# Optimization experiments

Measured on AMD Instinct MI355X. Metric: run time of the kernel, lower is better.

The kernel has to match this reference:

```python
import jax, jax.numpy as jnp
import numpy as np

B, Z, A = 1024, 512, 8          # batch_size, z_dim, action_dim
AH, ZH = 64, 512                # action_hidden_dim, z_hidden_dim
N_NEG = 100                     # n_neg_actions
TEMP = 0.1                      # temperature
TOP_K = (1, 3, 10)


def forward_model(z, a, Wa, ba, W1, b1, W2, b2):
    # MLP forward model with skip connection (z_delta=True):
    # embed action, concat with z, 2-layer MLP predicting a delta.
    h_a = jax.nn.relu(a @ Wa + ba)                                   # [..., AH]
    h = jax.nn.relu(jnp.concatenate([jnp.broadcast_to(z, a.shape[:-1] + (Z,)), h_a], axis=-1) @ W1 + b1)  # [..., ZH]
    delta = h @ W2 + b2                                              # [..., Z]
    return z + delta


def setup_inputs() -> dict:
    key = jax.random.key(0)
    ks = jax.random.split(key, 8)
    def w(k, shape, fan_in):
        return jax.random.normal(k, shape, jnp.float32) / np.float32(np.sqrt(fan_in))
    z = jax.random.normal(ks[0], (B, Z), jnp.float32)
    z_next = jax.random.normal(ks[1], (B, Z), jnp.float32)
    z_next_hat = jax.random.normal(ks[2], (B, Z), jnp.float32)
    actions = jax.random.normal(ks[3], (B, A), jnp.float32)
    Wa = w(ks[4], (A, AH), A)
    ba = jnp.zeros((AH,), jnp.float32)
    W1 = w(ks[5], (Z + AH, ZH), Z + AH)
    b1 = jnp.zeros((ZH,), jnp.float32)
    W2 = w(ks[6], (ZH, Z), ZH)
    b2 = jnp.zeros((Z,), jnp.float32)
    return {"z": z, "z_next": z_next, "z_next_hat": z_next_hat, "actions": actions,
            "Wa": Wa, "ba": ba, "W1": W1, "b1": b1, "W2": W2, "b2": b2}


def reference(z, z_next, z_next_hat, actions, Wa, ba, W1, b1, W2, b2):
    # ControlCPC.compute_loss with dot_product_similarity, vectorized:
    # the Python loop over n_neg_actions rolled-action forward-model calls
    # becomes one batched [n-1, B, ...] forward-model evaluation.
    batch = z.shape[0]
    n = min(N_NEG, batch)
    sim = z_next @ z_next_hat.T                                      # [B, B] positives on diagonal
    shifts = jnp.arange(1, n)
    neg_actions = jax.vmap(lambda i: jnp.roll(actions, -i, axis=0))(shifts)  # [n-1, B, A]
    z_hat_neg = forward_model(z[None], neg_actions, Wa, ba, W1, b1, W2, b2)  # [n-1, B, Z]
    neg_sim = jnp.einsum('nbz,bz->bn', z_hat_neg, z_next)            # diag of similarity per shift
    sim_mat = jnp.concatenate([sim, neg_sim], axis=1)                # [B, B+n-1]
    # INCE loss, positives on diagonal
    logp = jax.nn.log_softmax(sim_mat / jnp.float32(TEMP), axis=1)
    loss = -jnp.mean(jnp.diagonal(logp))                             # diagonal takes first B entries
    labels = jnp.arange(batch)[:, None]
    accs = []
    for k in TOP_K:
        _, preds = jax.lax.top_k(sim_mat, k)                         # [B, k]
        accs.append(jnp.mean((preds == labels).astype(jnp.float32)) * k)
    return (loss, accs[0], accs[1], accs[2])
```

## Files before the change

kernel.cpp:

```cpp
#include <hip/hip_runtime.h>
#include <math.h>

#define B_SZ 1024
#define Z_DIM 512
#define A_DIM 8
#define AH 64
#define ZH 512
#define NNEG 99
#define INV_T 10.0f

typedef __attribute__((ext_vector_type(8))) short short8;
typedef __attribute__((ext_vector_type(4))) short short4b;
typedef __attribute__((ext_vector_type(4))) float f32x4;

__device__ __forceinline__ short bf16rn(float x) {
    unsigned u = __float_as_uint(x);
    u += 0x7fffu + ((u >> 16) & 1u);
    return (short)(u >> 16);
}
__device__ __forceinline__ void cvt8rn(float4 x0, float4 x1, short8& h) {
    h[0] = bf16rn(x0.x); h[1] = bf16rn(x0.y); h[2] = bf16rn(x0.z); h[3] = bf16rn(x0.w);
    h[4] = bf16rn(x1.x); h[5] = bf16rn(x1.y); h[6] = bf16rn(x1.z); h[7] = bf16rn(x1.w);
}

__device__ __forceinline__ int sw(int m, int kb) { return m * 8 + (kb ^ (m & 7)); }

#define VMWAIT(N) asm volatile("s_waitcnt vmcnt(" #N ")" ::: "memory")
__device__ __forceinline__ void raw_barrier() {
    asm volatile("" ::: "memory");
    __builtin_amdgcn_s_barrier();
    asm volatile("" ::: "memory");
}
typedef const __attribute__((address_space(1))) void* gas_ptr;
typedef __attribute__((address_space(3))) void* las_ptr;
__device__ __forceinline__ void gld_lds16(const void* gsrc, void* ldst) {
    __builtin_amdgcn_global_load_lds((gas_ptr)gsrc, (las_ptr)ldst, 16, 0, 0);
}

__global__ __launch_bounds__(256) void cvt_kernel(
    const float* __restrict__ z, const float* __restrict__ z_next,
    const float* __restrict__ z_next_hat, const float* __restrict__ W1,
    const float* __restrict__ W2, const float* __restrict__ actions,
    const float* __restrict__ Wa, const float* __restrict__ ba,
    short* __restrict__ zb, short* __restrict__ znb, short* __restrict__ znhb,
    short* __restrict__ w1t, short* __restrict__ w2b, short* __restrict__ hab)
{
    const int id = blockIdx.x, tid = threadIdx.x;
    if (id < 896) {
        const float* src; short* dst; int local;
        if (id < 256)      { src = z;          dst = zb;   local = id; }
        else if (id < 512) { src = z_next;     dst = znb;  local = id - 256; }
        else if (id < 768) { src = z_next_hat; dst = znhb; local = id - 512; }
        else               { src = W2;         dst = w2b;  local = id - 768; }
        int i8 = local * 2048 + tid * 8;
        float4 x0 = *(const float4*)&src[i8];
        float4 x1 = *(const float4*)&src[i8 + 4];
        short8 h; cvt8rn(x0, x1, h);
        *(short8*)&dst[i8] = h;
    } else if (id < 968) {
        __shared__ float L[64][68];
        int local = id - 896, kt = local >> 3, nt = local & 7;
#pragma unroll
        for (int i = 0; i < 4; ++i) {
            int f = tid + i * 256;
            int r = f >> 4, c4 = (f & 15) << 2;
            *(float4*)&L[r][c4] = *(const float4*)&W1[(kt * 64 + r) * 512 + nt * 64 + c4];
        }
        __syncthreads();
#pragma unroll
        for (int i = 0; i < 4; ++i) {
            int f = tid + i * 256;
            int r = f >> 4, c4 = (f & 15) << 2;
            short4b o = {bf16rn(L[c4][r]), bf16rn(L[c4 + 1][r]),
                         bf16rn(L[c4 + 2][r]), bf16rn(L[c4 + 3][r])};
            *(short4b*)&w1t[(nt * 64 + r) * 576 + kt * 64 + c4] = o;
        }
    } else {
        __shared__ float sWa[A_DIM * 64];
        __shared__ float sba[64];
        int j0 = (id - 968) * 64;
        for (int i = tid; i < A_DIM * 64; i += 256) sWa[i] = Wa[i];
        if (tid < 64) sba[tid] = ba[tid];
        __syncthreads();
        int r = tid >> 2, c0 = (tid & 3) * 16;
        float4 a0 = *(const float4*)&actions[(j0 + r) * A_DIM + 0];
        float4 a1 = *(const float4*)&actions[(j0 + r) * A_DIM + 4];
        float av[8] = {a0.x, a0.y, a0.z, a0.w, a1.x, a1.y, a1.z, a1.w};
        float o[16];
#pragma unroll
        for (int c = 0; c < 16; ++c) o[c] = sba[c0 + c];
#pragma unroll
        for (int k = 0; k < A_DIM; ++k)
#pragma unroll
            for (int c = 0; c < 16; ++c) o[c] += av[k] * sWa[k * 64 + c0 + c];
#pragma unroll
        for (int c = 0; c < 16; c += 4) {
            short4b h = {bf16rn(fmaxf(o[c], 0.f)),     bf16rn(fmaxf(o[c + 1], 0.f)),
                         bf16rn(fmaxf(o[c + 2], 0.f)), bf16rn(fmaxf(o[c + 3], 0.f))};
            *(short4b*)&hab[(j0 + r) * 64 + c0 + c] = h;
        }
    }
}

__global__ __launch_bounds__(256, 2) void mm_kernel(
    const short* __restrict__ zb, const short* __restrict__ znb,
    const short* __restrict__ znhb, const short* __restrict__ w1t,
    const short* __restrict__ w2b, const short* __restrict__ hab,
    const float* __restrict__ b1,
    float* __restrict__ sim, float* __restrict__ u, float* __restrict__ v,
    float* __restrict__ g)
{
    __shared__ __align__(16) short Ah[128 * 64], Bh[128 * 64];

    const int id = blockIdx.x;
    const int tid = threadIdx.x;

    const short* A; const short* B; const float* bias = nullptr;
    float* C; int N, K, lda, ldb, bm0, bn0;
    if (id < 64) {
        bm0 = (id >> 3) * 128; bn0 = (id & 7) * 128;
        A = znb; lda = 512; B = znhb; ldb = 512; C = sim; N = 1024; K = 512;
    } else if (id < 96) {
        int t = id - 64; bm0 = (t >> 2) * 128; bn0 = (t & 3) * 128;
        A = zb; lda = 512; B = w1t; ldb = 576; C = u; N = 512; K = 512; bias = b1;
    } else if (id < 128) {
        int t = id - 96; bm0 = (t >> 2) * 128; bn0 = (t & 3) * 128;
        A = znb; lda = 512; B = w2b; ldb = 512; C = v; N = 512; K = 512;
    } else {
        int t = id - 128; bm0 = (t >> 2) * 128; bn0 = (t & 3) * 128;
        A = hab; lda = 64; B = w1t + 512; ldb = 576; C = g; N = 512; K = 64;
    }

    const int lane = tid & 63, wv = tid >> 6;
    const int lm = lane & 15, lq = lane >> 4;
    const int wr = (wv >> 1) * 64, wc = (wv & 1) * 64;
    short8* A8 = (short8*)Ah; short8* B8 = (short8*)Bh;
    f32x4 acc[4][4] = {};

    for (int k0 = 0; k0 < K; k0 += 64) {
#pragma unroll
        for (int q = 0; q < 4; ++q) {
            int f = q * 256 + tid;
            int row = f >> 3;
            int ug = (f & 7) ^ (row & 7);
            gld_lds16(&A[(bm0 + row) * lda + k0 + ug * 8],
                      &Ah[(q * 256 + wv * 64) * 8]);
            gld_lds16(&B[(bn0 + row) * ldb + k0 + ug * 8],
                      &Bh[(q * 256 + wv * 64) * 8]);
        }
        VMWAIT(0);
        raw_barrier();
#pragma unroll
        for (int kk = 0; kk < 64; kk += 32) {
            int kbi = (kk >> 3) + lq;
            short8 ah[4], bh[4];
#pragma unroll
            for (int i = 0; i < 4; ++i) ah[i] = A8[sw(wr + i * 16 + lm, kbi)];
#pragma unroll
            for (int j = 0; j < 4; ++j) bh[j] = B8[sw(wc + j * 16 + lm, kbi)];
#pragma unroll
            for (int i = 0; i < 4; ++i)
#pragma unroll
                for (int j = 0; j < 4; ++j)
                    acc[i][j] = __builtin_amdgcn_mfma_f32_16x16x32_bf16(ah[i], bh[j], acc[i][j], 0, 0, 0);
        }
        raw_barrier();
    }
#pragma unroll
    for (int i = 0; i < 4; ++i)
#pragma unroll
        for (int j = 0; j < 4; ++j) {
            int n = bn0 + wc + j * 16 + lm;
            float bb = bias ? bias[n] : 0.0f;
#pragma unroll
            for (int r = 0; r < 4; ++r) {
                int m = bm0 + wr + i * 16 + lq * 4 + r;
                C[m * N + n] = acc[i][j][r] + bb;
            }
        }
}

#define LOADC(GA, GB, kk) { \
    const int q0_ = (kk) * 8; \
    _Pragma("unroll") \
    for (int c_ = 0; c_ < 8; ++c_) { \
        int j_ = (b + 1 + q0_ + c_) & (B_SZ - 1); \
        GA[c_] = *(const float4*)&g[j_ * 512 + lane * 4]; \
        GB[c_] = *(const float4*)&g[j_ * 512 + 256 + lane * 4]; \
    } }

#define LOADC3(GA, GB) { \
    _Pragma("unroll") \
    for (int c_ = 0; c_ < 3; ++c_) { \
        int j_ = (b + 97 + c_) & (B_SZ - 1); \
        GA[c_] = *(const float4*)&g[j_ * 512 + lane * 4]; \
        GB[c_] = *(const float4*)&g[j_ * 512 + 256 + lane * 4]; \
    } }

#define DOTC(T, GA, GB, NC) { \
    _Pragma("unroll") \
    for (int c_ = 0; c_ < (NC); ++c_) { \
        float s_ = 0.0f; \
        s_ += fmaxf(ua.x + GA[c_].x, 0.0f) * va.x; \
        s_ += fmaxf(ua.y + GA[c_].y, 0.0f) * va.y; \
        s_ += fmaxf(ua.z + GA[c_].z, 0.0f) * va.z; \
        s_ += fmaxf(ua.w + GA[c_].w, 0.0f) * va.w; \
        s_ += fmaxf(ub.x + GB[c_].x, 0.0f) * vb.x; \
        s_ += fmaxf(ub.y + GB[c_].y, 0.0f) * vb.y; \
        s_ += fmaxf(ub.z + GB[c_].z, 0.0f) * vb.z; \
        s_ += fmaxf(ub.w + GB[c_].w, 0.0f) * vb.w; \
        T[c_] = s_; \
    } }

#define REDST(T, kk, NC) { \
    for (int off_ = 32; off_; off_ >>= 1) { \
        _Pragma("unroll") \
        for (int c_ = 0; c_ < (NC); ++c_) T[c_] += __shfl_down(T[c_], off_); \
    } \
    if (lane == 0) { \
        _Pragma("unroll") \
        for (int c_ = 0; c_ < (NC); ++c_) rn[(kk) * 8 + c_] = c0 + T[c_]; \
    } }

__global__ __launch_bounds__(256, 2) void row2_kernel(
    const float* __restrict__ sim, const float* __restrict__ u,
    const float* __restrict__ v, const float* __restrict__ g,
    const float* __restrict__ z, const float* __restrict__ z_next,
    const float* __restrict__ b2,
    float* __restrict__ pw)
{
    const int b = blockIdx.x;
    const int tid = threadIdx.x;
    const int w = tid >> 6, lane = tid & 63;
    __shared__ float rn[104];
    __shared__ float sred[12];

    float4 ua = *(const float4*)&u[b * 512 + lane * 4];
    float4 ub = *(const float4*)&u[b * 512 + 256 + lane * 4];
    float4 va = *(const float4*)&v[b * 512 + lane * 4];
    float4 vb = *(const float4*)&v[b * 512 + 256 + lane * 4];
    float4 s4 = *(const float4*)&sim[b * 1024 + tid * 4];
    float diag = sim[b * 1024 + b];

    float p;
    {
        float4 za = *(const float4*)&z[b * 512 + lane * 4];
        float4 zb4 = *(const float4*)&z[b * 512 + 256 + lane * 4];
        float4 na = *(const float4*)&z_next[b * 512 + lane * 4];
        float4 nb = *(const float4*)&z_next[b * 512 + 256 + lane * 4];
        float4 ca = *(const float4*)&b2[lane * 4];
        float4 cb = *(const float4*)&b2[256 + lane * 4];
        p  = (za.x + ca.x) * na.x + (za.y + ca.y) * na.y + (za.z + ca.z) * na.z + (za.w + ca.w) * na.w;
        p += (zb4.x + cb.x) * nb.x + (zb4.y + cb.y) * nb.y + (zb4.z + cb.z) * nb.z + (zb4.w + cb.w) * nb.w;
    }
    for (int off = 32; off; off >>= 1) p += __shfl_down(p, off);
    const float c0 = __shfl(p, 0);

    {
        const int k0 = w, k1 = w + 4, k2 = w + 8;
        float4 gaA[8], gbA[8], gaB[8], gbB[8];
        float tA[8], tB[8];

        LOADC(gaA, gbA, k0);
        LOADC(gaB, gbB, k1);
        DOTC(tA, gaA, gbA, 8);
        LOADC(gaA, gbA, k2);
        REDST(tA, k0, 8);
        DOTC(tB, gaB, gbB, 8);
        if (w == 0) LOADC3(gaB, gbB);
        REDST(tB, k1, 8);
        DOTC(tA, gaA, gbA, 8);
        REDST(tA, k2, 8);
        if (w == 0) {
            DOTC(tB, gaB, gbB, 3);
            REDST(tB, 12, 3);
        }
    }
    __syncthreads();

    float neg = (tid < NNEG) ? rn[tid] : -3.4e38f;

    float m = fmaxf(fmaxf(s4.x, s4.y), fmaxf(s4.z, s4.w));
    m = fmaxf(m, neg);
    for (int off = 32; off; off >>= 1) m = fmaxf(m, __shfl_xor(m, off));
    if (lane == 0) sred[w] = m;
    __syncthreads();
    m = fmaxf(fmaxf(sred[0], sred[1]), fmaxf(sred[2], sred[3]));

    float es = 0.0f; int ck = 0;
    {
        float xs[4] = {s4.x, s4.y, s4.z, s4.w};
#pragma unroll
        for (int c = 0; c < 4; ++c) {
            int j = tid * 4 + c;
            float x = xs[c];
            es += __expf((x - m) * INV_T);
            if (x > diag) ck++;
            else if (j < b && x == diag) ck++;
        }
    }
    if (tid < NNEG) {
        es += __expf((neg - m) * INV_T);
        if (neg > diag) ck++;
    }
    float ckf = (float)ck;
    for (int off = 32; off; off >>= 1) {
        es += __shfl_down(es, off);
        ckf += __shfl_down(ckf, off);
    }
    if (lane == 0) { sred[4 + w] = es; sred[8 + w] = ckf; }
    __syncthreads();
    if (tid == 0) {
        float est = sred[4] + sred[5] + sred[6] + sred[7];
        int ckt = (int)(sred[8] + sred[9] + sred[10] + sred[11]);
        pw[b * 4 + 0] = (m - diag) * INV_T + logf(est);
        pw[b * 4 + 1] = (ckt < 1) ? 1.0f : 0.0f;
        pw[b * 4 + 2] = (ckt < 3) ? 1.0f : 0.0f;
        pw[b * 4 + 3] = (ckt < 10) ? 1.0f : 0.0f;
    }
}

__global__ __launch_bounds__(256) void final_kernel(
    const float* __restrict__ pw, float* __restrict__ out)
{
    __shared__ float red[256];
    const int tid = threadIdx.x;
    const int c = tid & 3;
    float s = 0.0f;
    for (int r = tid >> 2; r < 1024; r += 64) s += pw[r * 4 + c];
    red[tid] = s;
    __syncthreads();
    if (tid < 4) {
        float t = 0.0f;
        for (int q = 0; q < 64; ++q) t += red[tid + q * 4];
        out[tid] = t * (1.0f / (float)B_SZ);
    }
}

extern "C" void kernel_launch(void* const* d_in, const int* in_sizes, int n_in,
                              void* d_out, int out_size, void* d_ws, size_t ws_size,
                              hipStream_t stream) {
    const float* z          = (const float*)d_in[0];
    const float* z_next     = (const float*)d_in[1];
    const float* z_next_hat = (const float*)d_in[2];
    const float* actions    = (const float*)d_in[3];
    const float* Wa         = (const float*)d_in[4];
    const float* ba         = (const float*)d_in[5];
    const float* W1         = (const float*)d_in[6];
    const float* b1         = (const float*)d_in[7];
    const float* W2         = (const float*)d_in[8];
    const float* b2         = (const float*)d_in[9];
    float* out = (float*)d_out;

    float* ws   = (float*)d_ws;
    float* sim  = ws;
    float* u    = sim + B_SZ * B_SZ;
    float* v    = u + B_SZ * ZH;
    float* g    = v + B_SZ * ZH;
    float* pw   = g + B_SZ * ZH;
    short* zb   = (short*)(pw + B_SZ * 4);
    short* znb  = zb + B_SZ * Z_DIM;
    short* znhb = znb + B_SZ * Z_DIM;
    short* w1t  = znhb + B_SZ * Z_DIM;
    short* w2b  = w1t + 512 * 576;
    short* hab  = w2b + 512 * 512;

    cvt_kernel<<<984, 256, 0, stream>>>(z, z_next, z_next_hat, W1, W2,
                                        actions, Wa, ba,
                                        zb, znb, znhb, w1t, w2b, hab);
    mm_kernel<<<160, 256, 0, stream>>>(zb, znb, znhb, w1t, w2b, hab, b1,
                                       sim, u, v, g);
    row2_kernel<<<1024, 256, 0, stream>>>(sim, u, v, g, z, z_next, b2, pw);
    final_kernel<<<1, 256, 0, stream>>>(pw, out);
}
```

Baseline: 115.2 us.

## Split row kernel into a wide negative-score kernel and a separate softmax kernel

Moves the 99 rolled-action negative dot products out of the per-row kernel into a new 2D-grid kernel with 1024x13 single-wave blocks, each handling 8 shifts. Scores go to a workspace buffer, and a separate softmax/top-k kernel reads them and adds the skip-connection constant. The aim is more parallelism and better latency hiding for the gather-heavy negative computation. The cost is an extra kernel launch and a round trip of the scores through global memory.

```diff
diff --git a/kernel.cpp b/kernel.cpp
--- a/kernel.cpp
+++ b/kernel.cpp
@@ -8,6 +8,7 @@
 #define ZH 512
 #define NNEG 99
 #define INV_T 10.0f
+#define RNP 104
 
 typedef __attribute__((ext_vector_type(8))) short short8;
 typedef __attribute__((ext_vector_type(4))) short short4b;
@@ -180,105 +181,76 @@
         }
 }
 
-#define LOADC(GA, GB, kk) { \
-    const int q0_ = (kk) * 8; \
-    _Pragma("unroll") \
-    for (int c_ = 0; c_ < 8; ++c_) { \
-        int j_ = (b + 1 + q0_ + c_) & (B_SZ - 1); \
-        GA[c_] = *(const float4*)&g[j_ * 512 + lane * 4]; \
-        GB[c_] = *(const float4*)&g[j_ * 512 + 256 + lane * 4]; \
-    } }
-
-#define LOADC3(GA, GB) { \
-    _Pragma("unroll") \
-    for (int c_ = 0; c_ < 3; ++c_) { \
-        int j_ = (b + 97 + c_) & (B_SZ - 1); \
-        GA[c_] = *(const float4*)&g[j_ * 512 + lane * 4]; \
-        GB[c_] = *(const float4*)&g[j_ * 512 + 256 + lane * 4]; \
-    } }
-
-#define DOTC(T, GA, GB, NC) { \
-    _Pragma("unroll") \
-    for (int c_ = 0; c_ < (NC); ++c_) { \
-        float s_ = 0.0f; \
-        s_ += fmaxf(ua.x + GA[c_].x, 0.0f) * va.x; \
-        s_ += fmaxf(ua.y + GA[c_].y, 0.0f) * va.y; \
-        s_ += fmaxf(ua.z + GA[c_].z, 0.0f) * va.z; \
-        s_ += fmaxf(ua.w + GA[c_].w, 0.0f) * va.w; \
-        s_ += fmaxf(ub.x + GB[c_].x, 0.0f) * vb.x; \
-        s_ += fmaxf(ub.y + GB[c_].y, 0.0f) * vb.y; \
-        s_ += fmaxf(ub.z + GB[c_].z, 0.0f) * vb.z; \
-        s_ += fmaxf(ub.w + GB[c_].w, 0.0f) * vb.w; \
-        T[c_] = s_; \
-    } }
-
-#define REDST(T, kk, NC) { \
-    for (int off_ = 32; off_; off_ >>= 1) { \
-        _Pragma("unroll") \
-        for (int c_ = 0; c_ < (NC); ++c_) T[c_] += __shfl_down(T[c_], off_); \
-    } \
-    if (lane == 0) { \
-        _Pragma("unroll") \
-        for (int c_ = 0; c_ < (NC); ++c_) rn[(kk) * 8 + c_] = c0 + T[c_]; \
-    } }
-
-__global__ __launch_bounds__(256, 2) void row2_kernel(
-    const float* __restrict__ sim, const float* __restrict__ u,
-    const float* __restrict__ v, const float* __restrict__ g,
-    const float* __restrict__ z, const float* __restrict__ z_next,
-    const float* __restrict__ b2,
-    float* __restrict__ pw)
-{
-    const int b = blockIdx.x;
-    const int tid = threadIdx.x;
-    const int w = tid >> 6, lane = tid & 63;
-    __shared__ float rn[104];
-    __shared__ float sred[12];
-
+__global__ __launch_bounds__(64, 4) void neg_kernel(
+    const float* __restrict__ u, const float* __restrict__ v,
+    const float* __restrict__ g, float* __restrict__ rnall)
+{
+    const int b = blockIdx.x, t = blockIdx.y;
+    const int lane = threadIdx.x;
+    const int s0 = 1 + t * 8;
+
+    float4 ga[8], gb[8];
+#pragma unroll
+    for (int c = 0; c < 8; ++c) {
+        int j = (b + s0 + c) & (B_SZ - 1);
+        ga[c] = *(const float4*)&g[j * 512 + lane * 4];
+        gb[c] = *(const float4*)&g[j * 512 + 256 + lane * 4];
+    }
     float4 ua = *(const float4*)&u[b * 512 + lane * 4];
     float4 ub = *(const float4*)&u[b * 512 + 256 + lane * 4];
     float4 va = *(const float4*)&v[b * 512 + lane * 4];
     float4 vb = *(const float4*)&v[b * 512 + 256 + lane * 4];
+
+    float d[8];
+#pragma unroll
+    for (int c = 0; c < 8; ++c) {
+        float s = 0.0f;
+        s += fmaxf(ua.x + ga[c].x, 0.0f) * va.x;
+        s += fmaxf(ua.y + ga[c].y, 0.0f) * va.y;
+        s += fmaxf(ua.z + ga[c].z, 0.0f) * va.z;
+        s += fmaxf(ua.w + ga[c].w, 0.0f) * va.w;
+        s += fmaxf(ub.x + gb[c].x, 0.0f) * vb.x;
+        s += fmaxf(ub.y + gb[c].y, 0.0f) * vb.y;
+        s += fmaxf(ub.z + gb[c].z, 0.0f) * vb.z;
+        s += fmaxf(ub.w + gb[c].w, 0.0f) * vb.w;
+        d[c] = s;
+    }
+    for (int off = 32; off; off >>= 1) {
+#pragma unroll
+        for (int c = 0; c < 8; ++c) d[c] += __shfl_down(d[c], off);
+    }
+    if (lane == 0) {
+#pragma unroll
+        for (int c = 0; c < 8; ++c)
+            if (s0 + c <= NNEG) rnall[b * RNP + s0 + c - 1] = d[c];
+    }
+}
+
+__global__ __launch_bounds__(256) void smax_kernel(
+    const float* __restrict__ sim, const float* __restrict__ rnall,
+    const float* __restrict__ z, const float* __restrict__ z_next,
+    const float* __restrict__ b2, float* __restrict__ pw)
+{
+    const int b = blockIdx.x;
+    const int tid = threadIdx.x;
+    const int w = tid >> 6, lane = tid & 63;
+    __shared__ float sred[12];
+
     float4 s4 = *(const float4*)&sim[b * 1024 + tid * 4];
+    float rawn = (tid < NNEG) ? rnall[b * RNP + tid] : 0.0f;
     float diag = sim[b * 1024 + b];
 
-    float p;
-    {
-        float4 za = *(const float4*)&z[b * 512 + lane * 4];
-        float4 zb4 = *(const float4*)&z[b * 512 + 256 + lane * 4];
-        float4 na = *(const float4*)&z_next[b * 512 + lane * 4];
-        float4 nb = *(const float4*)&z_next[b * 512 + 256 + lane * 4];
-        float4 ca = *(const float4*)&b2[lane * 4];
-        float4 cb = *(const float4*)&b2[256 + lane * 4];
-        p  = (za.x + ca.x) * na.x + (za.y + ca.y) * na.y + (za.z + ca.z) * na.z + (za.w + ca.w) * na.w;
-        p += (zb4.x + cb.x) * nb.x + (zb4.y + cb.y) * nb.y + (zb4.z + cb.z) * nb.z + (zb4.w + cb.w) * nb.w;
-    }
+    float2 z2 = *(const float2*)&z[b * 512 + tid * 2];
+    float2 n2 = *(const float2*)&z_next[b * 512 + tid * 2];
+    float2 c2 = *(const float2*)&b2[tid * 2];
+    float p = (z2.x + c2.x) * n2.x + (z2.y + c2.y) * n2.y;
     for (int off = 32; off; off >>= 1) p += __shfl_down(p, off);
-    const float c0 = __shfl(p, 0);
-
-    {
-        const int k0 = w, k1 = w + 4, k2 = w + 8;
-        float4 gaA[8], gbA[8], gaB[8], gbB[8];
-        float tA[8], tB[8];
-
-        LOADC(gaA, gbA, k0);
-        LOADC(gaB, gbB, k1);
-        DOTC(tA, gaA, gbA, 8);
-        LOADC(gaA, gbA, k2);
-        REDST(tA, k0, 8);
-        DOTC(tB, gaB, gbB, 8);
-        if (w == 0) LOADC3(gaB, gbB);
-        REDST(tB, k1, 8);
-        DOTC(tA, gaA, gbA, 8);
-        REDST(tA, k2, 8);
-        if (w == 0) {
-            DOTC(tB, gaB, gbB, 3);
-            REDST(tB, 12, 3);
-        }
-    }
-    __syncthreads();
-
-    float neg = (tid < NNEG) ? rn[tid] : -3.4e38f;
+    if (lane == 0) sred[w] = p;
+    __syncthreads();
+    const float c0 = sred[0] + sred[1] + sred[2] + sred[3];
+    __syncthreads();
+
+    float neg = (tid < NNEG) ? (rawn + c0) : -3.4e38f;
 
     float m = fmaxf(fmaxf(s4.x, s4.y), fmaxf(s4.z, s4.w));
     m = fmaxf(m, neg);
@@ -352,24 +324,26 @@
     const float* b2         = (const float*)d_in[9];
     float* out = (float*)d_out;
 
-    float* ws   = (float*)d_ws;
-    float* sim  = ws;
-    float* u    = sim + B_SZ * B_SZ;
-    float* v    = u + B_SZ * ZH;
-    float* g    = v + B_SZ * ZH;
-    float* pw   = g + B_SZ * ZH;
-    short* zb   = (short*)(pw + B_SZ * 4);
-    short* znb  = zb + B_SZ * Z_DIM;
-    short* znhb = znb + B_SZ * Z_DIM;
-    short* w1t  = znhb + B_SZ * Z_DIM;
-    short* w2b  = w1t + 512 * 576;
-    short* hab  = w2b + 512 * 512;
+    float* ws    = (float*)d_ws;
+    float* sim   = ws;
+    float* u     = sim + B_SZ * B_SZ;
+    float* v     = u + B_SZ * ZH;
+    float* g     = v + B_SZ * ZH;
+    float* pw    = g + B_SZ * ZH;
+    float* rnall = pw + B_SZ * 4;
+    short* zb    = (short*)(rnall + B_SZ * RNP);
+    short* znb   = zb + B_SZ * Z_DIM;
+    short* znhb  = znb + B_SZ * Z_DIM;
+    short* w1t   = znhb + B_SZ * Z_DIM;
+    short* w2b   = w1t + 512 * 576;
+    short* hab   = w2b + 512 * 512;
 
     cvt_kernel<<<984, 256, 0, stream>>>(z, z_next, z_next_hat, W1, W2,
                                         actions, Wa, ba,
                                         zb, znb, znhb, w1t, w2b, hab);
     mm_kernel<<<160, 256, 0, stream>>>(zb, znb, znhb, w1t, w2b, hab, b1,
                                        sim, u, v, g);
-    row2_kernel<<<1024, 256, 0, stream>>>(sim, u, v, g, z, z_next, b2, pw);
+    neg_kernel<<<dim3(B_SZ, 13), 64, 0, stream>>>(u, v, g, rnall);
+    smax_kernel<<<B_SZ, 256, 0, stream>>>(sim, rnall, z, z_next, b2, pw);
     final_kernel<<<1, 256, 0, stream>>>(pw, out);
 }
```

New measurement: 114.2 us (median of 2 runs). No clear change (-0.9%).
